# Optimization experiments

Hardware: AMD Instinct MI355X
Metric: run time of the kernel (lower is better)

The kernel has to match this reference:

```python
import jax, jax.numpy as jnp
import numpy as np

B, T, D, H, HS = 2, 256, 2048, 32, 64
LORA, DLORA, ST = 32, 64, 66  # maa lora rank, decay lora rank, state rows (2+HS)
EPS = 1e-5


def setup_inputs() -> dict:
    key = jax.random.key(0)
    ks = jax.random.split(key, 24)
    n = lambda k, sh, s=0.02: (jax.random.normal(k, sh, jnp.float32) * s)
    u = lambda k, sh: jax.random.uniform(k, sh, jnp.float32)
    return {
        "x": jax.random.normal(ks[0], (B, T, D), jnp.float32),
        "state": jax.random.normal(ks[1], (B, ST, D), jnp.float32) * 0.1,
        "ln1_w": jnp.ones((D,), jnp.float32),
        "ln1_b": jnp.zeros((D,), jnp.float32),
        "time_maa_x": u(ks[2], (D,)),
        "time_maa_w1": n(ks[3], (D, 5 * LORA)),
        "time_maa_w2": n(ks[4], (5, LORA, D)),
        "time_maa_k": u(ks[5], (D,)),
        "time_maa_w": u(ks[6], (D,)),
        "time_maa_v": u(ks[7], (D,)),
        "time_maa_r": u(ks[8], (D,)),
        "time_maa_g": u(ks[9], (D,)),
        "time_decay": n(ks[10], (D,), 0.5),
        "time_decay_w1": n(ks[11], (D, DLORA)),
        "time_decay_w2": n(ks[12], (DLORA, D)),
        "time_faaaa": n(ks[13], (H, HS, 1), 0.1),
        "receptance_weight": n(ks[14], (D, D)),
        "key_weight": n(ks[15], (D, D)),
        "value_weight": n(ks[16], (D, D)),
        "output_weight": n(ks[17], (D, D)),
        "gate_weight": n(ks[18], (D, D)),
        "lnx_w": jnp.ones((D,), jnp.float32),
        "lnx_b": jnp.zeros((D,), jnp.float32),
        "i": 0,
    }


def reference(x, state, ln1_w, ln1_b, time_maa_x, time_maa_w1, time_maa_w2,
              time_maa_k, time_maa_w, time_maa_v, time_maa_r, time_maa_g,
              time_decay, time_decay_w1, time_decay_w2, time_faaaa,
              receptance_weight, key_weight, value_weight, output_weight,
              gate_weight, lnx_w, lnx_b, i):
    # forward() early-returns time_mixing(ln1(x), state, i)
    mu = x.mean(-1, keepdims=True)
    var = ((x - mu) ** 2).mean(-1, keepdims=True)
    x = (x - mu) * jax.lax.rsqrt(var + EPS) * ln1_w + ln1_b

    i1 = (2 + HS) * i + 1
    # token shift: sx[t] = x[t-1] - x[t], with state row i1 as x[-1]
    sx = jnp.concatenate([state[:, i1][:, None] - x[:, :1], x[:, :-1] - x[:, 1:]], axis=1)

    xxx = x + sx * time_maa_x
    t5 = jnp.tanh(xxx @ time_maa_w1).reshape(B, T, 5, LORA)
    xxx5 = jnp.einsum('btfr,frd->btfd', t5, time_maa_w2)          # [B,T,5,D]
    maa = jnp.stack([time_maa_k, time_maa_w, time_maa_v, time_maa_r, time_maa_g])  # [5,D]
    x5 = x[:, :, None] + sx[:, :, None] * (maa + xxx5)            # [B,T,5,D]

    k = (x5[:, :, 0] @ key_weight.T).reshape(B, T, H, HS)
    w = jnp.exp(-jnp.exp(time_decay + jnp.tanh(x5[:, :, 1] @ time_decay_w1) @ time_decay_w2)).reshape(B, T, H, HS)
    v = (x5[:, :, 2] @ value_weight.T).reshape(B, T, H, HS)
    r = (x5[:, :, 3] @ receptance_weight.T).reshape(B, T, H, HS)
    g = jax.nn.silu(x5[:, :, 4] @ gate_weight.T)                  # [B,T,D]

    kv = jnp.einsum('bthi,bthj->bthij', k, v)                     # [B,T,H,HS,HS]
    prev0 = state[:, i1 + 1:i1 + 1 + HS].reshape(B, H, HS, HS)

    def step(prev, xs):
        kv_t, w_t = xs
        return kv_t + w_t[..., None] * prev, prev  # emit state BEFORE update

    _, state_s = jax.lax.scan(step, prev0,
                              (kv.transpose(1, 0, 2, 3, 4), w.transpose(1, 0, 2, 3)))
    state_s = state_s.transpose(1, 0, 2, 3, 4)                    # [B,T,H,HS,HS]

    wkv = time_faaaa * kv + state_s
    rwkv = jnp.einsum('bthj,bthjd->bthd', r, wkv)                 # [B,T,H,HS]

    # GroupNorm(num_groups=H) over each head's HS channels
    gm = rwkv.mean(-1, keepdims=True)
    gv = ((rwkv - gm) ** 2).mean(-1, keepdims=True)
    normed = (rwkv - gm) * jax.lax.rsqrt(gv + EPS)
    normed = normed * lnx_w.reshape(H, HS) + lnx_b.reshape(H, HS)
    normed = normed.reshape(B, T, D)

    return (normed * g) @ output_weight.T
```

## Files before the change

### kernel.cpp

```cpp
#include <hip/hip_runtime.h>
#include <hip/hip_bf16.h>

typedef unsigned short u16;
typedef __attribute__((ext_vector_type(4))) float f32x4;
typedef __attribute__((ext_vector_type(8))) short short8;
typedef __attribute__((ext_vector_type(4))) short bf16x4;

#define B_ 2
#define T_ 256
#define D_ 2048
#define H_ 32
#define HS_ 64
#define M_ 512
#define ST_ 66
#define EPS_ 1e-5f

__device__ __forceinline__ float bf2f(u16 u) {
    union { unsigned int i; float f; } c; c.i = ((unsigned int)u) << 16; return c.f;
}
__device__ __forceinline__ u16 f2bf(float f) {
    union { unsigned int i; float f; } c; c.f = f;
    unsigned int r = c.i + 0x7fffu + ((c.i >> 16) & 1u);
    return (u16)(r >> 16);
}
__device__ __forceinline__ u16 f2bf_hw(float f) {
    __hip_bfloat16 b = __float2bfloat16(f);
    return *reinterpret_cast<u16*>(&b);
}

__global__ __launch_bounds__(256) void ln_kernel(const float* __restrict__ x, const float* __restrict__ w,
                                                 const float* __restrict__ bias, float* __restrict__ xln)
{
    const int row = blockIdx.x;
    const float* xr = x + (size_t)row * D_;
    float* orow = xln + (size_t)row * D_;
    const int t = threadIdx.x;
    f32x4 a0 = *(const f32x4*)(xr + t * 8);
    f32x4 a1 = *(const f32x4*)(xr + t * 8 + 4);
    float s = 0.f, q = 0.f;
#pragma unroll
    for (int i = 0; i < 4; i++) { s += a0[i] + a1[i]; q += a0[i]*a0[i] + a1[i]*a1[i]; }
#pragma unroll
    for (int off = 1; off < 64; off <<= 1) { s += __shfl_xor(s, off, 64); q += __shfl_xor(q, off, 64); }
    __shared__ float ls[4], lq[4];
    const int wid = t >> 6, lane = t & 63;
    if (lane == 0) { ls[wid] = s; lq[wid] = q; }
    __syncthreads();
    s = ls[0] + ls[1] + ls[2] + ls[3];
    q = lq[0] + lq[1] + lq[2] + lq[3];
    const float mu = s * (1.f / D_);
    const float var = q * (1.f / D_) - mu * mu;
    const float rs = rsqrtf(var + EPS_);
#pragma unroll
    for (int i = 0; i < 8; i++) {
        int d = t * 8 + i;
        float f = (i < 4) ? a0[i] : a1[i - 4];
        orow[d] = (f - mu) * rs * w[d] + bias[d];
    }
}

__global__ __launch_bounds__(256) void shift_kernel(const float* __restrict__ xln, const float* __restrict__ state,
                                                    const float* __restrict__ maax, const int* __restrict__ ip,
                                                    float* __restrict__ sx, u16* __restrict__ xxxb)
{
    const size_t gid = (size_t)blockIdx.x * 256 + threadIdx.x;
    const size_t e = gid * 4;
    const int row = (int)(e >> 11);
    const int d = (int)(e & 2047);
    const int tt = row & (T_ - 1);
    const int b = row >> 8;
    const float* prev;
    if (tt == 0) prev = state + ((size_t)b * ST_ + (size_t)(66 * ip[0] + 1)) * D_ + d;
    else         prev = xln + e - D_;
    f32x4 p = *(const f32x4*)prev;
    f32x4 c = *(const f32x4*)(xln + e);
    f32x4 mx = *(const f32x4*)(maax + d);
    f32x4 sv;
    bf16x4 xv;
#pragma unroll
    for (int i = 0; i < 4; i++) { sv[i] = p[i] - c[i]; xv[i] = (short)f2bf(c[i] + sv[i] * mx[i]); }
    *(f32x4*)(sx + e) = sv;
    *(bf16x4*)(xxxb + e) = xv;
}

__global__ __launch_bounds__(256) void txp_kernel(const float* __restrict__ in, u16* __restrict__ out,
                                                  int K, int N)
{
    __shared__ float tile[32][33];
    const int k0 = blockIdx.x * 32, n0 = blockIdx.y * 32;
    const int c = threadIdx.x & 31, r8 = threadIdx.x >> 5;
#pragma unroll
    for (int i = 0; i < 4; i++) {
        int r = r8 + i * 8;
        tile[r][c] = in[(size_t)(k0 + r) * N + (n0 + c)];
    }
    __syncthreads();
#pragma unroll
    for (int i = 0; i < 4; i++) {
        int r = r8 + i * 8;
        out[(size_t)(n0 + r) * K + (k0 + c)] = f2bf(tile[c][r]);
    }
}

template<int NN, bool TANH>
__global__ __launch_bounds__(256) void gsmall_kernel(const u16* __restrict__ A, const u16* __restrict__ Wt,
                                                     float* __restrict__ C, int ldc)
{
    __shared__ u16 As[128 * 32];
    __shared__ u16 Ws[64 * 32];
    const int tid = threadIdx.x;
    const int m0 = blockIdx.y * 128, n0 = blockIdx.x * 64;
    const int lane = tid & 63, wid = tid >> 6;
    const int wm = (wid >> 1) * 64, wn = (wid & 1) * 32;

    f32x4 acc[4][2];
#pragma unroll
    for (int i = 0; i < 4; i++)
#pragma unroll
        for (int j = 0; j < 2; j++) { acc[i][j][0]=0.f; acc[i][j][1]=0.f; acc[i][j][2]=0.f; acc[i][j][3]=0.f; }

    const int rA = tid >> 2;
    const int kA = (tid & 3) * 8;
    const u16* gA0 = A + (size_t)(m0 + rA) * D_ + kA;
    const u16* gA1 = A + (size_t)(m0 + rA + 64) * D_ + kA;
    int wrow = n0 + rA; if (wrow >= NN) wrow = NN - 1;
    const u16* gW = Wt + (size_t)wrow * D_ + kA;
    u16* lA0 = As + tid * 8;
    u16* lA1 = As + (tid + 256) * 8;
    u16* lW  = Ws + tid * 8;
    const u16* pa = As + (size_t)(wm + (lane & 15)) * 32 + (lane >> 4) * 8;
    const u16* pb = Ws + (size_t)(wn + (lane & 15)) * 32 + (lane >> 4) * 8;

    short8 a0 = *(const short8*)gA0;
    short8 a1 = *(const short8*)gA1;
    short8 w0 = *(const short8*)gW;

    for (int kt = 0; kt < D_; kt += 32) {
        const int kt2 = (kt + 32) & (D_ - 1);
        short8 na0 = *(const short8*)(gA0 + kt2);
        short8 na1 = *(const short8*)(gA1 + kt2);
        short8 nw0 = *(const short8*)(gW + kt2);
        __syncthreads();
        *(short8*)lA0 = a0;
        *(short8*)lA1 = a1;
        *(short8*)lW  = w0;
        __syncthreads();
        short8 av[4], bv[2];
#pragma unroll
        for (int mi = 0; mi < 4; mi++) av[mi] = *(const short8*)(pa + mi * 16 * 32);
#pragma unroll
        for (int ni = 0; ni < 2; ni++) bv[ni] = *(const short8*)(pb + ni * 16 * 32);
#pragma unroll
        for (int mi = 0; mi < 4; mi++)
#pragma unroll
            for (int ni = 0; ni < 2; ni++)
                acc[mi][ni] = __builtin_amdgcn_mfma_f32_16x16x32_bf16(av[mi], bv[ni], acc[mi][ni], 0, 0, 0);
        a0 = na0; a1 = na1; w0 = nw0;
    }
    const int cr = wm + (lane >> 4) * 4;
    const int cc = wn + (lane & 15);
#pragma unroll
    for (int mi = 0; mi < 4; mi++)
#pragma unroll
        for (int ni = 0; ni < 2; ni++) {
            const int col = n0 + cc + ni * 16;
            if (col < NN) {
#pragma unroll
                for (int j = 0; j < 4; j++) {
                    float v = acc[mi][ni][j];
                    if (TANH) v = tanhf(v);
                    C[(size_t)(m0 + cr + mi * 16 + j) * ldc + col] = v;
                }
            }
        }
}

__global__ __launch_bounds__(256) void maa2_kernel(const float* __restrict__ t5, const float* __restrict__ w2,
                                                   const float* __restrict__ xln, const float* __restrict__ sxp,
                                                   const float* __restrict__ mk, const float* __restrict__ mw,
                                                   const float* __restrict__ mv, const float* __restrict__ mr,
                                                   const float* __restrict__ mg, u16* __restrict__ x5)
{
    const int gid = blockIdx.x * 256 + threadIdx.x;
    const int d = gid & (D_ - 1);
    const int f = (gid >> 11) % 5;
    const int mg4 = gid / (5 * D_);
    const float* maa = (f == 0) ? mk : (f == 1) ? mw : (f == 2) ? mv : (f == 3) ? mr : mg;
    const float mf = maa[d];
    const float* w2f = w2 + (size_t)f * 32 * D_ + d;
    const float* t5b = t5 + (size_t)mg4 * 4 * 160 + f * 32;
    float a0 = 0, a1 = 0, a2 = 0, a3 = 0;
#pragma unroll 8
    for (int r = 0; r < 32; r++) {
        float wv = w2f[(size_t)r * D_];
        a0 = fmaf(t5b[r], wv, a0);
        a1 = fmaf(t5b[160 + r], wv, a1);
        a2 = fmaf(t5b[320 + r], wv, a2);
        a3 = fmaf(t5b[480 + r], wv, a3);
    }
    const float accs[4] = {a0, a1, a2, a3};
    const size_t m0 = (size_t)mg4 * 4;
#pragma unroll
    for (int mm = 0; mm < 4; mm++) {
        size_t e = (m0 + mm) * D_ + d;
        x5[(size_t)f * M_ * D_ + e] = f2bf(xln[e] + sxp[e] * (mf + accs[mm]));
    }
}

__global__ __launch_bounds__(256) void decay2_kernel(const float* __restrict__ td, const float* __restrict__ dw2,
                                                     const float* __restrict__ tdec, float* __restrict__ wout)
{
    const int gid = blockIdx.x * 256 + threadIdx.x;
    const int d = gid & (D_ - 1);
    const int mg4 = gid >> 11;
    const float* wp = dw2 + d;
    const float* tb = td + (size_t)mg4 * 4 * 64;
    float a0 = 0, a1 = 0, a2 = 0, a3 = 0;
#pragma unroll 8
    for (int r = 0; r < 64; r++) {
        float wv = wp[(size_t)r * D_];
        a0 = fmaf(tb[r], wv, a0);
        a1 = fmaf(tb[64 + r], wv, a1);
        a2 = fmaf(tb[128 + r], wv, a2);
        a3 = fmaf(tb[192 + r], wv, a3);
    }
    const float base = tdec[d];
    const float accs[4] = {a0, a1, a2, a3};
#pragma unroll
    for (int mm = 0; mm < 4; mm++)
        wout[((size_t)mg4 * 4 + mm) * D_ + d] = expf(-expf(base + accs[mm]));
}

#define LDP_ 40
__device__ __forceinline__ void gemm64_body(const u16* __restrict__ A, const float* __restrict__ W,
                                            float* __restrict__ C)
{
    __shared__ u16 As[64 * LDP_];
    __shared__ u16 Bs[64 * LDP_];
    const int tid = threadIdx.x;
    const int m0 = blockIdx.y * 64;
    const int n0 = blockIdx.x * 64;
    const int lane = tid & 63;
    const int wid = tid >> 6;
    const int wm = (wid >> 1) * 32;
    const int wn = (wid & 1) * 32;

    f32x4 acc[2][2];
#pragma unroll
    for (int i = 0; i < 2; i++)
#pragma unroll
        for (int j = 0; j < 2; j++) { acc[i][j][0]=0.f; acc[i][j][1]=0.f; acc[i][j][2]=0.f; acc[i][j][3]=0.f; }

    const int rA = tid >> 2;
    const int kc = (tid & 3) * 8;
    const u16* gA = A + (size_t)(m0 + rA) * D_ + kc;
    const float* gW = W + (size_t)(n0 + rA) * D_ + kc;
    u16* lA = As + rA * LDP_ + kc;
    u16* lB = Bs + rA * LDP_ + kc;
    const u16* pa = As + (size_t)(wm + (lane & 15)) * LDP_ + (lane >> 4) * 8;
    const u16* pb = Bs + (size_t)(wn + (lane & 15)) * LDP_ + (lane >> 4) * 8;

    short8 a0 = *(const short8*)gA;
    f32x4 w0 = *(const f32x4*)gW;
    f32x4 w1 = *(const f32x4*)(gW + 4);

    for (int kt = 0; kt < D_; kt += 32) {
        const int kt2 = (kt + 32) & (D_ - 1);
        short8 na = *(const short8*)(gA + kt2);
        f32x4 nw0 = *(const f32x4*)(gW + kt2);
        f32x4 nw1 = *(const f32x4*)(gW + kt2 + 4);
        __syncthreads();
        *(short8*)lA = a0;
        short8 sb;
#pragma unroll
        for (int j = 0; j < 4; j++) {
            sb[j]     = (short)f2bf_hw(w0[j]);
            sb[j + 4] = (short)f2bf_hw(w1[j]);
        }
        *(short8*)lB = sb;
        __syncthreads();
        short8 av[2], bv[2];
#pragma unroll
        for (int mi = 0; mi < 2; mi++) av[mi] = *(const short8*)(pa + mi * 16 * LDP_);
#pragma unroll
        for (int ni = 0; ni < 2; ni++) bv[ni] = *(const short8*)(pb + ni * 16 * LDP_);
#pragma unroll
        for (int mi = 0; mi < 2; mi++)
#pragma unroll
            for (int ni = 0; ni < 2; ni++)
                acc[mi][ni] = __builtin_amdgcn_mfma_f32_16x16x32_bf16(av[mi], bv[ni], acc[mi][ni], 0, 0, 0);
        a0 = na; w0 = nw0; w1 = nw1;
    }
    const int cr = wm + (lane >> 4) * 4;
    const int cc = wn + (lane & 15);
#pragma unroll
    for (int mi = 0; mi < 2; mi++)
#pragma unroll
        for (int ni = 0; ni < 2; ni++)
#pragma unroll
            for (int j = 0; j < 4; j++)
                C[(size_t)(m0 + cr + mi * 16 + j) * D_ + (n0 + cc + ni * 16)] = acc[mi][ni][j];
}

__global__ __launch_bounds__(256) void gemm4_kernel(const u16* __restrict__ x5, const float* __restrict__ Wk,
                                                    const float* __restrict__ Wv, const float* __restrict__ Wr,
                                                    const float* __restrict__ Wg, float* __restrict__ kvrg)
{
    const int mm = blockIdx.z;
    const u16* A = x5 + (size_t)(mm == 0 ? 0 : mm + 1) * M_ * D_;
    const float* W = (mm == 0) ? Wk : (mm == 1) ? Wv : (mm == 2) ? Wr : Wg;
    float* C = kvrg + (size_t)mm * M_ * D_;
    gemm64_body(A, W, C);
}

__global__ __launch_bounds__(256) void gemm1_kernel(const u16* __restrict__ y, const float* __restrict__ Wo,
                                                    float* __restrict__ out)
{
    gemm64_body(y, Wo, out);
}

#define CH_ 16
__global__ __launch_bounds__(512) void rec_kernel(const float* __restrict__ rB, const float* __restrict__ kB,
                                                  const float* __restrict__ wB, const float* __restrict__ vB,
                                                  const float* __restrict__ fa, const float* __restrict__ state,
                                                  const int* __restrict__ ip, float* __restrict__ rwkv)
{
    const int bh = blockIdx.x;
    const int b = bh >> 5, h = bh & 31;
    const int tid = threadIdx.x;
    const int wv = tid >> 6, lane = tid & 63;
    const int wg = wv >> 2;
    const int jb = lane >> 3, dsub = lane & 7;
    const int jbase = jb * 8;
    const int d0 = wg * 32 + (wv & 3) * 8 + dsub;

    __shared__ float stage[2][4][CH_][64];
    __shared__ float p2[CH_][8][64];
    __shared__ float p1[CH_][8];

    float S[8], faj[8];
    {
        const float* Sp = state + (size_t)b * ST_ * D_ + (size_t)(66 * ip[0] + 2) * D_ + (size_t)h * HS_ * HS_;
#pragma unroll
        for (int jj = 0; jj < 8; jj++) {
            S[jj]   = Sp[(jbase + jj) * 64 + d0];
            faj[jj] = fa[h * 64 + jbase + jj];
        }
    }
    const size_t base = ((size_t)b * T_ * H_ + h) * HS_;
    const int arr = wv & 3;
    const float* mysrc = (arr == 0) ? rB : (arr == 1) ? kB : (arr == 2) ? wB : vB;
    const int ts0 = wg * 8 + (lane >> 4);
    const int sch = (lane & 15) * 4;
    const bool p1w = (wv == 0 && dsub == 0);

    f32x4 pre[2];
#pragma unroll
    for (int p = 0; p < 2; p++)
        pre[p] = *(const f32x4*)(mysrc + base + (size_t)(ts0 + p * 4) * (H_ * HS_) + sch);
#pragma unroll
    for (int p = 0; p < 2; p++)
        *(f32x4*)&stage[0][arr][ts0 + p * 4][sch] = pre[p];
    __syncthreads();

    int cb = 0;
    for (int c = 0; c < T_ / CH_; ++c) {
        const bool more = (c + 1 < T_ / CH_);
        if (more) {
#pragma unroll
            for (int p = 0; p < 2; p++)
                pre[p] = *(const f32x4*)(mysrc + base + (size_t)((c + 1) * CH_ + ts0 + p * 4) * (H_ * HS_) + sch);
        }
        f32x4 r0 = *(const f32x4*)&stage[cb][0][0][jbase];
        f32x4 r1 = *(const f32x4*)&stage[cb][0][0][jbase + 4];
        f32x4 k0 = *(const f32x4*)&stage[cb][1][0][jbase];
        f32x4 k1 = *(const f32x4*)&stage[cb][1][0][jbase + 4];
        f32x4 w0 = *(const f32x4*)&stage[cb][2][0][jbase];
        f32x4 w1 = *(const f32x4*)&stage[cb][2][0][jbase + 4];
        float vd = stage[cb][3][0][d0];
#pragma unroll
        for (int ts = 0; ts < CH_; ++ts) {
            f32x4 nr0 = r0, nr1 = r1, nk0 = k0, nk1 = k1, nw0 = w0, nw1 = w1;
            float nvd = vd;
            if (ts + 1 < CH_) {
                nr0 = *(const f32x4*)&stage[cb][0][ts + 1][jbase];
                nr1 = *(const f32x4*)&stage[cb][0][ts + 1][jbase + 4];
                nk0 = *(const f32x4*)&stage[cb][1][ts + 1][jbase];
                nk1 = *(const f32x4*)&stage[cb][1][ts + 1][jbase + 4];
                nw0 = *(const f32x4*)&stage[cb][2][ts + 1][jbase];
                nw1 = *(const f32x4*)&stage[cb][2][ts + 1][jbase + 4];
                nvd = stage[cb][3][ts + 1][d0];
            }
            float s1 = 0.f, s2 = 0.f;
#pragma unroll
            for (int q = 0; q < 4; q++) {
                s1 = fmaf(r0[q] * faj[q],     k0[q], s1);
                s1 = fmaf(r1[q] * faj[q + 4], k1[q], s1);
                s2 = fmaf(r0[q], S[q],     s2);
                s2 = fmaf(r1[q], S[q + 4], s2);
            }
            p2[ts][jb][d0 ^ (jb << 3)] = s2;
            if (p1w) p1[ts][jb] = s1;
#pragma unroll
            for (int q = 0; q < 4; q++) {
                S[q]     = fmaf(w0[q], S[q],     k0[q] * vd);
                S[q + 4] = fmaf(w1[q], S[q + 4], k1[q] * vd);
            }
            r0 = nr0; r1 = nr1; k0 = nk0; k1 = nk1; w0 = nw0; w1 = nw1; vd = nvd;
        }
        if (more) {
#pragma unroll
            for (int p = 0; p < 2; p++)
                *(f32x4*)&stage[cb ^ 1][arr][ts0 + p * 4][sch] = pre[p];
        }
        __syncthreads();
#pragma unroll
        for (int p = 0; p < 2; p++) {
            const int ts = wv * 2 + p;
            f32x4 p1a = *(const f32x4*)&p1[ts][0];
            f32x4 p1b = *(const f32x4*)&p1[ts][4];
            float s1t = ((p1a[0] + p1a[1]) + (p1a[2] + p1a[3])) +
                        ((p1b[0] + p1b[1]) + (p1b[2] + p1b[3]));
            float s2t = 0.f;
#pragma unroll
            for (int j = 0; j < 8; j++) s2t += p2[ts][j][lane ^ (j << 3)];
            const float vvv = stage[cb][3][ts][lane];
            rwkv[base + (size_t)(c * CH_ + ts) * (H_ * HS_) + lane] = fmaf(vvv, s1t, s2t);
        }
        __syncthreads();
        cb ^= 1;
    }
}

__global__ __launch_bounds__(256) void gn_kernel(const float* __restrict__ rwkv, const float* __restrict__ gpre,
                                                 const float* __restrict__ lnxw, const float* __restrict__ lnxb,
                                                 u16* __restrict__ y)
{
    const int g = blockIdx.x * 4 + (threadIdx.x >> 6);
    const int lane = threadIdx.x & 63;
    const size_t e = (size_t)g * 64 + lane;
    const float val = rwkv[e];
    float s = val, q = val * val;
#pragma unroll
    for (int off = 1; off < 64; off <<= 1) { s += __shfl_xor(s, off, 64); q += __shfl_xor(q, off, 64); }
    const float mu = s * (1.f / 64.f);
    const float var = q * (1.f / 64.f) - mu * mu;
    const float rs = rsqrtf(var + EPS_);
    const int hj = (int)(e & (size_t)(D_ - 1));
    const float nrm = (val - mu) * rs * lnxw[hj] + lnxb[hj];
    const float gp = gpre[e];
    const float gv = gp / (1.f + expf(-gp));
    y[e] = f2bf(nrm * gv);
}

extern "C" void kernel_launch(void* const* d_in, const int* in_sizes, int n_in,
                              void* d_out, int out_size, void* d_ws, size_t ws_size,
                              hipStream_t stream)
{
    const float* x     = (const float*)d_in[0];
    const float* state = (const float*)d_in[1];
    const float* ln1w  = (const float*)d_in[2];
    const float* ln1b  = (const float*)d_in[3];
    const float* maax  = (const float*)d_in[4];
    const float* w1    = (const float*)d_in[5];
    const float* w2    = (const float*)d_in[6];
    const float* maak  = (const float*)d_in[7];
    const float* maaw  = (const float*)d_in[8];
    const float* maav  = (const float*)d_in[9];
    const float* maar  = (const float*)d_in[10];
    const float* maag  = (const float*)d_in[11];
    const float* tdec  = (const float*)d_in[12];
    const float* dw1   = (const float*)d_in[13];
    const float* dw2   = (const float*)d_in[14];
    const float* fa    = (const float*)d_in[15];
    const float* wrec  = (const float*)d_in[16];
    const float* wkey  = (const float*)d_in[17];
    const float* wval  = (const float*)d_in[18];
    const float* wout  = (const float*)d_in[19];
    const float* wgate = (const float*)d_in[20];
    const float* lnxw  = (const float*)d_in[21];
    const float* lnxb  = (const float*)d_in[22];
    const int*   ip    = (const int*)d_in[23];

    char* ws = (char*)d_ws;
    const size_t MD = (size_t)M_ * D_;
    float* xln  = (float*)(ws);
    float* sx   = (float*)(ws + ((size_t)4  << 20));
    u16*   xxxb = (u16*)  (ws + ((size_t)8  << 20));
    u16*   w1t  = (u16*)  (ws + ((size_t)10 << 20));
    u16*   dw1t = (u16*)  (ws + ((size_t)11 << 20));
    float* t5   = (float*)(ws + ((size_t)12 << 20));
    u16*   x5   = (u16*)  (ws + ((size_t)13 << 20));
    float* td   = (float*)(ws + ((size_t)23 << 20));
    float* wdec = (float*)(ws + ((size_t)24 << 20));
    float* kvrg = (float*)(ws + ((size_t)28 << 20));
    float* rwkv = (float*)(ws + ((size_t)44 << 20));
    u16*   y    = (u16*)  (ws + ((size_t)48 << 20));
    float* out  = (float*)d_out;

    hipLaunchKernelGGL(ln_kernel,     dim3(512),      dim3(256), 0, stream, x, ln1w, ln1b, xln);
    hipLaunchKernelGGL(shift_kernel,  dim3(1024),     dim3(256), 0, stream, xln, state, maax, ip, sx, xxxb);
    hipLaunchKernelGGL(txp_kernel,    dim3(64, 5),    dim3(256), 0, stream, w1, w1t, D_, 160);
    hipLaunchKernelGGL(txp_kernel,    dim3(64, 2),    dim3(256), 0, stream, dw1, dw1t, D_, 64);
    hipLaunchKernelGGL((gsmall_kernel<160, true>), dim3(3, 4), dim3(256), 0, stream, xxxb, w1t, t5, 160);
    hipLaunchKernelGGL(maa2_kernel,   dim3(5120),     dim3(256), 0, stream, t5, w2, xln, sx, maak, maaw, maav, maar, maag, x5);
    hipLaunchKernelGGL((gsmall_kernel<64, true>),  dim3(1, 4), dim3(256), 0, stream, x5 + MD, dw1t, td, 64);
    hipLaunchKernelGGL(decay2_kernel, dim3(1024),     dim3(256), 0, stream, td, dw2, tdec, wdec);
    hipLaunchKernelGGL(gemm4_kernel,  dim3(32, 8, 4), dim3(256), 0, stream, x5, wkey, wval, wrec, wgate, kvrg);
    hipLaunchKernelGGL(rec_kernel,    dim3(64),       dim3(512), 0, stream, kvrg + 2 * MD, kvrg, wdec, kvrg + MD, fa, state, ip, rwkv);
    hipLaunchKernelGGL(gn_kernel,     dim3(4096),     dim3(256), 0, stream, rwkv, kvrg + 3 * MD, lnxw, lnxb, y);
    hipLaunchKernelGGL(gemm1_kernel,  dim3(32, 8, 1), dim3(256), 0, stream, y, wout, out);

    (void)in_sizes; (void)n_in; (void)out_size; (void)ws_size;
}
```

Measured before the change: 214.8 us.

## Use 128x128 GEMM tiles with split-K and deeper prefetch

Replaces the 64x64-tile bf16 MFMA GEMM with a 128x128 tile on 512 threads, with each wave computing 32x64. It also prefetches two K-steps ahead instead of one. Both GEMM stages are split along K into partials (2-way for the k/v/r/g projections, 4-way for the output projection) and summed by separate elementwise add kernels, which keeps the grid large despite the bigger tiles. The aim is to cut redundant global reads of A and the fp32 weights and to raise MFMA work per LDS sync. The costs are extra partial-sum traffic plus two added kernel launches, and removing the LDS row padding may cause bank conflicts.

```diff
diff --git a/kernel.cpp b/kernel.cpp
--- a/kernel.cpp
+++ b/kernel.cpp
@@ -231,92 +231,122 @@
         wout[((size_t)mg4 * 4 + mm) * D_ + d] = expf(-expf(base + accs[mm]));
 }
 
-#define LDP_ 40
-__device__ __forceinline__ void gemm64_body(const u16* __restrict__ A, const float* __restrict__ W,
-                                            float* __restrict__ C)
-{
-    __shared__ u16 As[64 * LDP_];
-    __shared__ u16 Bs[64 * LDP_];
+__device__ __forceinline__ void gemm128_body(const u16* __restrict__ A, const float* __restrict__ W,
+                                             float* __restrict__ C, int k0, int KC)
+{
+    __shared__ u16 As[128 * 32];
+    __shared__ u16 Bs[128 * 32];
     const int tid = threadIdx.x;
-    const int m0 = blockIdx.y * 64;
-    const int n0 = blockIdx.x * 64;
+    const int m0 = blockIdx.y * 128;
+    const int n0 = blockIdx.x * 128;
     const int lane = tid & 63;
-    const int wid = tid >> 6;
-    const int wm = (wid >> 1) * 32;
-    const int wn = (wid & 1) * 32;
-
-    f32x4 acc[2][2];
+    const int wvid = tid >> 6;
+    const int wm = (wvid >> 1) * 32;
+    const int wn = (wvid & 1) * 64;
+
+    f32x4 acc[2][4];
 #pragma unroll
     for (int i = 0; i < 2; i++)
 #pragma unroll
-        for (int j = 0; j < 2; j++) { acc[i][j][0]=0.f; acc[i][j][1]=0.f; acc[i][j][2]=0.f; acc[i][j][3]=0.f; }
+        for (int j = 0; j < 4; j++) { acc[i][j][0]=0.f; acc[i][j][1]=0.f; acc[i][j][2]=0.f; acc[i][j][3]=0.f; }
 
     const int rA = tid >> 2;
     const int kc = (tid & 3) * 8;
-    const u16* gA = A + (size_t)(m0 + rA) * D_ + kc;
-    const float* gW = W + (size_t)(n0 + rA) * D_ + kc;
-    u16* lA = As + rA * LDP_ + kc;
-    u16* lB = Bs + rA * LDP_ + kc;
-    const u16* pa = As + (size_t)(wm + (lane & 15)) * LDP_ + (lane >> 4) * 8;
-    const u16* pb = Bs + (size_t)(wn + (lane & 15)) * LDP_ + (lane >> 4) * 8;
+    const u16* gA = A + (size_t)(m0 + rA) * D_ + k0 + kc;
+    const float* gW = W + (size_t)(n0 + rA) * D_ + k0 + kc;
+    u16* lA = As + rA * 32 + kc;
+    u16* lB = Bs + rA * 32 + kc;
+    const u16* pa = As + (size_t)(wm + (lane & 15)) * 32 + (lane >> 4) * 8;
+    const u16* pb = Bs + (size_t)(wn + (lane & 15)) * 32 + (lane >> 4) * 8;
 
     short8 a0 = *(const short8*)gA;
-    f32x4 w0 = *(const f32x4*)gW;
-    f32x4 w1 = *(const f32x4*)(gW + 4);
-
-    for (int kt = 0; kt < D_; kt += 32) {
-        const int kt2 = (kt + 32) & (D_ - 1);
-        short8 na = *(const short8*)(gA + kt2);
-        f32x4 nw0 = *(const f32x4*)(gW + kt2);
-        f32x4 nw1 = *(const f32x4*)(gW + kt2 + 4);
+    f32x4 w00 = *(const f32x4*)gW, w01 = *(const f32x4*)(gW + 4);
+    const int kt1 = (32 < KC) ? 32 : 0;
+    short8 a1 = *(const short8*)(gA + kt1);
+    f32x4 w10 = *(const f32x4*)(gW + kt1), w11 = *(const f32x4*)(gW + kt1 + 4);
+
+    for (int kt = 0; kt < KC; kt += 32) {
+        const int ktn = (kt + 64 < KC) ? kt + 64 : 0;
+        short8 an = *(const short8*)(gA + ktn);
+        f32x4 pw0 = *(const f32x4*)(gW + ktn), pw1 = *(const f32x4*)(gW + ktn + 4);
         __syncthreads();
         *(short8*)lA = a0;
         short8 sb;
 #pragma unroll
         for (int j = 0; j < 4; j++) {
-            sb[j]     = (short)f2bf_hw(w0[j]);
-            sb[j + 4] = (short)f2bf_hw(w1[j]);
+            sb[j]     = (short)f2bf_hw(w00[j]);
+            sb[j + 4] = (short)f2bf_hw(w01[j]);
         }
         *(short8*)lB = sb;
         __syncthreads();
-        short8 av[2], bv[2];
-#pragma unroll
-        for (int mi = 0; mi < 2; mi++) av[mi] = *(const short8*)(pa + mi * 16 * LDP_);
-#pragma unroll
-        for (int ni = 0; ni < 2; ni++) bv[ni] = *(const short8*)(pb + ni * 16 * LDP_);
+        short8 av[2], bv[4];
+#pragma unroll
+        for (int mi = 0; mi < 2; mi++) av[mi] = *(const short8*)(pa + mi * 16 * 32);
+#pragma unroll
+        for (int ni = 0; ni < 4; ni++) bv[ni] = *(const short8*)(pb + ni * 16 * 32);
 #pragma unroll
         for (int mi = 0; mi < 2; mi++)
 #pragma unroll
-            for (int ni = 0; ni < 2; ni++)
+            for (int ni = 0; ni < 4; ni++)
                 acc[mi][ni] = __builtin_amdgcn_mfma_f32_16x16x32_bf16(av[mi], bv[ni], acc[mi][ni], 0, 0, 0);
-        a0 = na; w0 = nw0; w1 = nw1;
+        a0 = a1; w00 = w10; w01 = w11;
+        a1 = an; w10 = pw0; w11 = pw1;
     }
     const int cr = wm + (lane >> 4) * 4;
     const int cc = wn + (lane & 15);
 #pragma unroll
     for (int mi = 0; mi < 2; mi++)
 #pragma unroll
-        for (int ni = 0; ni < 2; ni++)
+        for (int ni = 0; ni < 4; ni++)
 #pragma unroll
             for (int j = 0; j < 4; j++)
                 C[(size_t)(m0 + cr + mi * 16 + j) * D_ + (n0 + cc + ni * 16)] = acc[mi][ni][j];
 }
 
-__global__ __launch_bounds__(256) void gemm4_kernel(const u16* __restrict__ x5, const float* __restrict__ Wk,
-                                                    const float* __restrict__ Wv, const float* __restrict__ Wr,
-                                                    const float* __restrict__ Wg, float* __restrict__ kvrg)
-{
-    const int mm = blockIdx.z;
-    const u16* A = x5 + (size_t)(mm == 0 ? 0 : mm + 1) * M_ * D_;
-    const float* W = (mm == 0) ? Wk : (mm == 1) ? Wv : (mm == 2) ? Wr : Wg;
-    float* C = kvrg + (size_t)mm * M_ * D_;
-    gemm64_body(A, W, C);
-}
-
-__global__ __launch_bounds__(256) void gemm1_kernel(const u16* __restrict__ y, const float* __restrict__ Wo,
-                                                    float* __restrict__ out)
-{
-    gemm64_body(y, Wo, out);
+__global__ __launch_bounds__(512) void gemm4ks_kernel(const u16* __restrict__ x5, const float* __restrict__ Wk,
+                                                      const float* __restrict__ Wv, const float* __restrict__ Wr,
+                                                      const float* __restrict__ Wg, float* __restrict__ kvrg,
+                                                      float* __restrict__ pp, int KS)
+{
+    const int slice = blockIdx.z / KS;
+    const int ks = blockIdx.z - slice * KS;
+    const u16* A = x5 + (size_t)(slice == 0 ? 0 : slice + 1) * M_ * D_;
+    const float* W = (slice == 0) ? Wk : (slice == 1) ? Wv : (slice == 2) ? Wr : Wg;
+    float* C = (ks == 0) ? kvrg + (size_t)slice * M_ * D_ : pp + (size_t)slice * M_ * D_;
+    const int KC = D_ / KS;
+    gemm128_body(A, W, C, ks * KC, KC);
+}
+
+__global__ __launch_bounds__(512) void gemm1ks_kernel(const u16* __restrict__ y, const float* __restrict__ Wo,
+                                                      float* __restrict__ out, float* __restrict__ pp, int KS)
+{
+    const int ks = blockIdx.z;
+    float* C = (ks == 0) ? out : pp + (size_t)(ks - 1) * M_ * D_;
+    const int KC = D_ / KS;
+    gemm128_body(y, Wo, C, ks * KC, KC);
+}
+
+__global__ __launch_bounds__(256) void add1_kernel(float* __restrict__ dst, const float* __restrict__ s0)
+{
+    const size_t e = ((size_t)blockIdx.x * 256 + threadIdx.x) * 4;
+    f32x4 d = *(const f32x4*)(dst + e);
+    f32x4 a = *(const f32x4*)(s0 + e);
+#pragma unroll
+    for (int i = 0; i < 4; i++) d[i] += a[i];
+    *(f32x4*)(dst + e) = d;
+}
+
+__global__ __launch_bounds__(256) void add3_kernel(float* __restrict__ dst, const float* __restrict__ s0,
+                                                   const float* __restrict__ s1, const float* __restrict__ s2)
+{
+    const size_t e = ((size_t)blockIdx.x * 256 + threadIdx.x) * 4;
+    f32x4 d = *(const f32x4*)(dst + e);
+    f32x4 a = *(const f32x4*)(s0 + e);
+    f32x4 b = *(const f32x4*)(s1 + e);
+    f32x4 c = *(const f32x4*)(s2 + e);
+#pragma unroll
+    for (int i = 0; i < 4; i++) d[i] += (a[i] + b[i]) + c[i];
+    *(f32x4*)(dst + e) = d;
 }
 
 #define CH_ 16
@@ -496,7 +526,13 @@
     float* kvrg = (float*)(ws + ((size_t)28 << 20));
     float* rwkv = (float*)(ws + ((size_t)44 << 20));
     u16*   y    = (u16*)  (ws + ((size_t)48 << 20));
+    float* pp4  = (float*)(ws + ((size_t)50 << 20));
+    float* pp1  = (float*)(ws + ((size_t)66 << 20));
     float* out  = (float*)d_out;
+
+    const bool doks = ws_size >= ((size_t)78 << 20);
+    const int KS4 = doks ? 2 : 1;
+    const int KS1 = doks ? 4 : 1;
 
     hipLaunchKernelGGL(ln_kernel,     dim3(512),      dim3(256), 0, stream, x, ln1w, ln1b, xln);
     hipLaunchKernelGGL(shift_kernel,  dim3(1024),     dim3(256), 0, stream, xln, state, maax, ip, sx, xxxb);
@@ -506,10 +542,14 @@
     hipLaunchKernelGGL(maa2_kernel,   dim3(5120),     dim3(256), 0, stream, t5, w2, xln, sx, maak, maaw, maav, maar, maag, x5);
     hipLaunchKernelGGL((gsmall_kernel<64, true>),  dim3(1, 4), dim3(256), 0, stream, x5 + MD, dw1t, td, 64);
     hipLaunchKernelGGL(decay2_kernel, dim3(1024),     dim3(256), 0, stream, td, dw2, tdec, wdec);
-    hipLaunchKernelGGL(gemm4_kernel,  dim3(32, 8, 4), dim3(256), 0, stream, x5, wkey, wval, wrec, wgate, kvrg);
+    hipLaunchKernelGGL(gemm4ks_kernel, dim3(16, 4, 4 * KS4), dim3(512), 0, stream, x5, wkey, wval, wrec, wgate, kvrg, pp4, KS4);
+    if (doks)
+        hipLaunchKernelGGL(add1_kernel, dim3(4096), dim3(256), 0, stream, kvrg, pp4);
     hipLaunchKernelGGL(rec_kernel,    dim3(64),       dim3(512), 0, stream, kvrg + 2 * MD, kvrg, wdec, kvrg + MD, fa, state, ip, rwkv);
     hipLaunchKernelGGL(gn_kernel,     dim3(4096),     dim3(256), 0, stream, rwkv, kvrg + 3 * MD, lnxw, lnxb, y);
-    hipLaunchKernelGGL(gemm1_kernel,  dim3(32, 8, 1), dim3(256), 0, stream, y, wout, out);
-
-    (void)in_sizes; (void)n_in; (void)out_size; (void)ws_size;
-}
+    hipLaunchKernelGGL(gemm1ks_kernel, dim3(16, 4, KS1), dim3(512), 0, stream, y, wout, out, pp1, KS1);
+    if (doks)
+        hipLaunchKernelGGL(add3_kernel, dim3(1024), dim3(256), 0, stream, out, pp1, pp1 + MD, pp1 + 2 * MD);
+
+    (void)in_sizes; (void)n_in; (void)out_size;
+}
```

Result: faster. 203.1 us (-5.4%).

## Pre-convert weights to bf16, use async LDS-loading double-buffered GEMM with split-K output

Applied to the files above, without the earlier changes.

Adds a kernel that converts the five DxD fp32 weight matrices to bf16 once per call. The GEMMs are rewritten to use global_load_lds direct-to-LDS copies with double buffering, XOR-swizzled 128x64 tiles and a 64-wide K step. The output projection is split four ways along K, and an add kernel sums the partials. This removes per-tile fp32-to-bf16 conversion and register staging inside the GEMM, and raises parallelism for the last GEMM. In exchange it adds a full weight-conversion pass each call, extra launches and partial-sum traffic, and reuses workspace regions.

```diff
diff --git a/kernel.cpp b/kernel.cpp
--- a/kernel.cpp
+++ b/kernel.cpp
@@ -23,9 +23,25 @@
     unsigned int r = c.i + 0x7fffu + ((c.i >> 16) & 1u);
     return (u16)(r >> 16);
 }
-__device__ __forceinline__ u16 f2bf_hw(float f) {
-    __hip_bfloat16 b = __float2bfloat16(f);
-    return *reinterpret_cast<u16*>(&b);
+
+__device__ __forceinline__ void gld16(const u16* g, u16* l) {
+    __builtin_amdgcn_global_load_lds((const __attribute__((address_space(1))) void*)g,
+                                     (__attribute__((address_space(3))) void*)l, 16, 0, 0);
+}
+
+__global__ __launch_bounds__(256) void wcvt_kernel(const float* __restrict__ wk, const float* __restrict__ wv,
+                                                   const float* __restrict__ wr, const float* __restrict__ wg,
+                                                   const float* __restrict__ wo, u16* __restrict__ out)
+{
+    const int wsel = blockIdx.y;
+    const float* in = (wsel == 0) ? wk : (wsel == 1) ? wv : (wsel == 2) ? wr : (wsel == 3) ? wg : wo;
+    const size_t e = ((size_t)blockIdx.x * 256 + threadIdx.x) * 8;
+    f32x4 a = *(const f32x4*)(in + e);
+    f32x4 b = *(const f32x4*)(in + e + 4);
+    short8 o;
+#pragma unroll
+    for (int i = 0; i < 4; i++) { o[i] = (short)f2bf(a[i]); o[i + 4] = (short)f2bf(b[i]); }
+    *(short8*)(out + (size_t)wsel * D_ * D_ + e) = o;
 }
 
 __global__ __launch_bounds__(256) void ln_kernel(const float* __restrict__ x, const float* __restrict__ w,
@@ -231,70 +247,72 @@
         wout[((size_t)mg4 * 4 + mm) * D_ + d] = expf(-expf(base + accs[mm]));
 }
 
-#define LDP_ 40
-__device__ __forceinline__ void gemm64_body(const u16* __restrict__ A, const float* __restrict__ W,
-                                            float* __restrict__ C)
-{
-    __shared__ u16 As[64 * LDP_];
-    __shared__ u16 Bs[64 * LDP_];
+__device__ __forceinline__ void gemm2p_body(const u16* __restrict__ A, const u16* __restrict__ Wb,
+                                            float* __restrict__ C, int m0, int n0, int k0, int KC)
+{
+    __shared__ u16 As[2][128 * 64];
+    __shared__ u16 Bs[2][64 * 64];
     const int tid = threadIdx.x;
-    const int m0 = blockIdx.y * 64;
-    const int n0 = blockIdx.x * 64;
     const int lane = tid & 63;
-    const int wid = tid >> 6;
-    const int wm = (wid >> 1) * 32;
-    const int wn = (wid & 1) * 32;
-
-    f32x4 acc[2][2];
-#pragma unroll
-    for (int i = 0; i < 2; i++)
+    const int wvd = tid >> 6;
+    const int wm = (wvd >> 1) * 64;
+    const int wn = (wvd & 1) * 32;
+
+    f32x4 acc[4][2];
+#pragma unroll
+    for (int i = 0; i < 4; i++)
 #pragma unroll
         for (int j = 0; j < 2; j++) { acc[i][j][0]=0.f; acc[i][j][1]=0.f; acc[i][j][2]=0.f; acc[i][j][3]=0.f; }
 
-    const int rA = tid >> 2;
-    const int kc = (tid & 3) * 8;
-    const u16* gA = A + (size_t)(m0 + rA) * D_ + kc;
-    const float* gW = W + (size_t)(n0 + rA) * D_ + kc;
-    u16* lA = As + rA * LDP_ + kc;
-    u16* lB = Bs + rA * LDP_ + kc;
-    const u16* pa = As + (size_t)(wm + (lane & 15)) * LDP_ + (lane >> 4) * 8;
-    const u16* pb = Bs + (size_t)(wn + (lane & 15)) * LDP_ + (lane >> 4) * 8;
-
-    short8 a0 = *(const short8*)gA;
-    f32x4 w0 = *(const f32x4*)gW;
-    f32x4 w1 = *(const f32x4*)(gW + 4);
-
-    for (int kt = 0; kt < D_; kt += 32) {
-        const int kt2 = (kt + 32) & (D_ - 1);
-        short8 na = *(const short8*)(gA + kt2);
-        f32x4 nw0 = *(const f32x4*)(gW + kt2);
-        f32x4 nw1 = *(const f32x4*)(gW + kt2 + 4);
+    const int srow = tid >> 3;
+    const int sw8  = (((tid & 7) ^ (srow & 7)) << 3);
+    const u16* Ag = A + (size_t)(m0 + srow) * D_ + k0 + sw8;
+    const u16* Wg = Wb + (size_t)(n0 + srow) * D_ + k0 + sw8;
+    const int ldst = tid * 8;
+
+    const int rsw = (lane & 7) << 3;
+    const int colb = (lane >> 4) * 8;
+    const int fr = lane & 15;
+
+#define STAGE_(bb, kt)                                                            \
+    {                                                                             \
+        _Pragma("unroll")                                                         \
+        for (int i = 0; i < 4; i++)                                               \
+            gld16(Ag + (size_t)(i * 32) * D_ + (kt), &As[bb][i * 2048 + ldst]);   \
+        _Pragma("unroll")                                                         \
+        for (int i = 0; i < 2; i++)                                               \
+            gld16(Wg + (size_t)(i * 32) * D_ + (kt), &Bs[bb][i * 2048 + ldst]);   \
+    }
+
+    STAGE_(0, 0);
+    __syncthreads();
+    int cur = 0;
+    for (int kt = 0; kt < KC; kt += 64) {
+        if (kt + 64 < KC) STAGE_(cur ^ 1, kt + 64);
+#pragma unroll
+        for (int kk = 0; kk < 64; kk += 32) {
+            const int c = (kk + colb) ^ rsw;
+            short8 av[4], bv[2];
+#pragma unroll
+            for (int mi = 0; mi < 4; mi++)
+                av[mi] = *(const short8*)&As[cur][(wm + mi * 16 + fr) * 64 + c];
+#pragma unroll
+            for (int ni = 0; ni < 2; ni++)
+                bv[ni] = *(const short8*)&Bs[cur][(wn + ni * 16 + fr) * 64 + c];
+#pragma unroll
+            for (int mi = 0; mi < 4; mi++)
+#pragma unroll
+                for (int ni = 0; ni < 2; ni++)
+                    acc[mi][ni] = __builtin_amdgcn_mfma_f32_16x16x32_bf16(av[mi], bv[ni], acc[mi][ni], 0, 0, 0);
+        }
         __syncthreads();
-        *(short8*)lA = a0;
-        short8 sb;
-#pragma unroll
-        for (int j = 0; j < 4; j++) {
-            sb[j]     = (short)f2bf_hw(w0[j]);
-            sb[j + 4] = (short)f2bf_hw(w1[j]);
-        }
-        *(short8*)lB = sb;
-        __syncthreads();
-        short8 av[2], bv[2];
-#pragma unroll
-        for (int mi = 0; mi < 2; mi++) av[mi] = *(const short8*)(pa + mi * 16 * LDP_);
-#pragma unroll
-        for (int ni = 0; ni < 2; ni++) bv[ni] = *(const short8*)(pb + ni * 16 * LDP_);
-#pragma unroll
-        for (int mi = 0; mi < 2; mi++)
-#pragma unroll
-            for (int ni = 0; ni < 2; ni++)
-                acc[mi][ni] = __builtin_amdgcn_mfma_f32_16x16x32_bf16(av[mi], bv[ni], acc[mi][ni], 0, 0, 0);
-        a0 = na; w0 = nw0; w1 = nw1;
-    }
+        cur ^= 1;
+    }
+#undef STAGE_
     const int cr = wm + (lane >> 4) * 4;
-    const int cc = wn + (lane & 15);
-#pragma unroll
-    for (int mi = 0; mi < 2; mi++)
+    const int cc = wn + fr;
+#pragma unroll
+    for (int mi = 0; mi < 4; mi++)
 #pragma unroll
         for (int ni = 0; ni < 2; ni++)
 #pragma unroll
@@ -302,21 +320,37 @@
                 C[(size_t)(m0 + cr + mi * 16 + j) * D_ + (n0 + cc + ni * 16)] = acc[mi][ni][j];
 }
 
-__global__ __launch_bounds__(256) void gemm4_kernel(const u16* __restrict__ x5, const float* __restrict__ Wk,
-                                                    const float* __restrict__ Wv, const float* __restrict__ Wr,
-                                                    const float* __restrict__ Wg, float* __restrict__ kvrg)
-{
-    const int mm = blockIdx.z;
-    const u16* A = x5 + (size_t)(mm == 0 ? 0 : mm + 1) * M_ * D_;
-    const float* W = (mm == 0) ? Wk : (mm == 1) ? Wv : (mm == 2) ? Wr : Wg;
-    float* C = kvrg + (size_t)mm * M_ * D_;
-    gemm64_body(A, W, C);
-}
-
-__global__ __launch_bounds__(256) void gemm1_kernel(const u16* __restrict__ y, const float* __restrict__ Wo,
-                                                    float* __restrict__ out)
-{
-    gemm64_body(y, Wo, out);
+__global__ __launch_bounds__(256) void gemm4g_kernel(const u16* __restrict__ x5, const u16* __restrict__ wcvt,
+                                                     float* __restrict__ kvK, float* __restrict__ kvV,
+                                                     float* __restrict__ kvR, float* __restrict__ kvG)
+{
+    const int s = blockIdx.z;
+    const u16* A = x5 + (size_t)(s == 0 ? 0 : s + 1) * M_ * D_;
+    const u16* W = wcvt + (size_t)s * D_ * D_;
+    float* C = (s == 0) ? kvK : (s == 1) ? kvV : (s == 2) ? kvR : kvG;
+    gemm2p_body(A, W, C, blockIdx.y * 128, blockIdx.x * 64, 0, D_);
+}
+
+__global__ __launch_bounds__(256) void gemm1g_kernel(const u16* __restrict__ y, const u16* __restrict__ wo,
+                                                     float* __restrict__ out, float* __restrict__ p0,
+                                                     float* __restrict__ p1, float* __restrict__ p2)
+{
+    const int ks = blockIdx.z;
+    float* C = (ks == 0) ? out : (ks == 1) ? p0 : (ks == 2) ? p1 : p2;
+    gemm2p_body(y, wo, C, blockIdx.y * 128, blockIdx.x * 64, ks * 512, 512);
+}
+
+__global__ __launch_bounds__(256) void add3_kernel(float* __restrict__ dst, const float* __restrict__ s0,
+                                                   const float* __restrict__ s1, const float* __restrict__ s2)
+{
+    const size_t e = ((size_t)blockIdx.x * 256 + threadIdx.x) * 4;
+    f32x4 d = *(const f32x4*)(dst + e);
+    f32x4 a = *(const f32x4*)(s0 + e);
+    f32x4 b = *(const f32x4*)(s1 + e);
+    f32x4 c = *(const f32x4*)(s2 + e);
+#pragma unroll
+    for (int i = 0; i < 4; i++) d[i] += (a[i] + b[i]) + c[i];
+    *(f32x4*)(dst + e) = d;
 }
 
 #define CH_ 16
@@ -484,20 +518,28 @@
 
     char* ws = (char*)d_ws;
     const size_t MD = (size_t)M_ * D_;
-    float* xln  = (float*)(ws);
-    float* sx   = (float*)(ws + ((size_t)4  << 20));
-    u16*   xxxb = (u16*)  (ws + ((size_t)8  << 20));
-    u16*   w1t  = (u16*)  (ws + ((size_t)10 << 20));
-    u16*   dw1t = (u16*)  (ws + ((size_t)11 << 20));
-    float* t5   = (float*)(ws + ((size_t)12 << 20));
-    u16*   x5   = (u16*)  (ws + ((size_t)13 << 20));
-    float* td   = (float*)(ws + ((size_t)23 << 20));
-    float* wdec = (float*)(ws + ((size_t)24 << 20));
-    float* kvrg = (float*)(ws + ((size_t)28 << 20));
-    float* rwkv = (float*)(ws + ((size_t)44 << 20));
-    u16*   y    = (u16*)  (ws + ((size_t)48 << 20));
+    u16*   wcvt = (u16*)  (ws);
+    float* xln  = (float*)(ws + ((size_t)40 << 20));
+    float* sx   = (float*)(ws + ((size_t)44 << 20));
+    u16*   xxxb = (u16*)  (ws + ((size_t)48 << 20));
+    u16*   w1t  = (u16*)  (ws + ((size_t)50 << 20));
+    u16*   dw1t = (u16*)  (ws + ((size_t)51 << 20));
+    float* t5   = (float*)(ws + ((size_t)52 << 20));
+    float* td   = (float*)(ws + ((size_t)53 << 20));
+    u16*   x5   = (u16*)  (ws + ((size_t)54 << 20));
+    float* wdec = (float*)(ws + ((size_t)64 << 20));
+    float* kvK  = (float*)(ws + ((size_t)40 << 20));
+    float* kvV  = (float*)(ws + ((size_t)44 << 20));
+    float* kvR  = (float*)(ws + ((size_t)48 << 20));
+    float* kvG  = (float*)(ws + ((size_t)68 << 20));
+    float* rwkv = (float*)(ws + ((size_t)72 << 20));
+    u16*   y    = (u16*)  (ws + ((size_t)76 << 20));
+    float* pp0  = (float*)(ws + ((size_t)54 << 20));
+    float* pp1  = (float*)(ws + ((size_t)58 << 20));
+    float* pp2  = (float*)(ws + ((size_t)62 << 20));
     float* out  = (float*)d_out;
 
+    hipLaunchKernelGGL(wcvt_kernel,   dim3(2048, 5),  dim3(256), 0, stream, wkey, wval, wrec, wgate, wout, wcvt);
     hipLaunchKernelGGL(ln_kernel,     dim3(512),      dim3(256), 0, stream, x, ln1w, ln1b, xln);
     hipLaunchKernelGGL(shift_kernel,  dim3(1024),     dim3(256), 0, stream, xln, state, maax, ip, sx, xxxb);
     hipLaunchKernelGGL(txp_kernel,    dim3(64, 5),    dim3(256), 0, stream, w1, w1t, D_, 160);
@@ -506,10 +548,11 @@
     hipLaunchKernelGGL(maa2_kernel,   dim3(5120),     dim3(256), 0, stream, t5, w2, xln, sx, maak, maaw, maav, maar, maag, x5);
     hipLaunchKernelGGL((gsmall_kernel<64, true>),  dim3(1, 4), dim3(256), 0, stream, x5 + MD, dw1t, td, 64);
     hipLaunchKernelGGL(decay2_kernel, dim3(1024),     dim3(256), 0, stream, td, dw2, tdec, wdec);
-    hipLaunchKernelGGL(gemm4_kernel,  dim3(32, 8, 4), dim3(256), 0, stream, x5, wkey, wval, wrec, wgate, kvrg);
-    hipLaunchKernelGGL(rec_kernel,    dim3(64),       dim3(512), 0, stream, kvrg + 2 * MD, kvrg, wdec, kvrg + MD, fa, state, ip, rwkv);
-    hipLaunchKernelGGL(gn_kernel,     dim3(4096),     dim3(256), 0, stream, rwkv, kvrg + 3 * MD, lnxw, lnxb, y);
-    hipLaunchKernelGGL(gemm1_kernel,  dim3(32, 8, 1), dim3(256), 0, stream, y, wout, out);
+    hipLaunchKernelGGL(gemm4g_kernel, dim3(32, 4, 4), dim3(256), 0, stream, x5, wcvt, kvK, kvV, kvR, kvG);
+    hipLaunchKernelGGL(rec_kernel,    dim3(64),       dim3(512), 0, stream, kvR, kvK, wdec, kvV, fa, state, ip, rwkv);
+    hipLaunchKernelGGL(gn_kernel,     dim3(4096),     dim3(256), 0, stream, rwkv, kvG, lnxw, lnxb, y);
+    hipLaunchKernelGGL(gemm1g_kernel, dim3(32, 4, 4), dim3(256), 0, stream, y, wcvt + (size_t)4 * D_ * D_, out, pp0, pp1, pp2);
+    hipLaunchKernelGGL(add3_kernel,   dim3(1024),     dim3(256), 0, stream, out, pp0, pp1, pp2);
 
     (void)in_sizes; (void)n_in; (void)out_size; (void)ws_size;
 }
```

Measured after the change: 213.8 us. About the same (-0.5%).
